# Kernel optimization log

Hardware: AMD Instinct MI355X
Metric: run time of the kernel (lower is better)

The kernel has to match this reference:

```python
import jax, jax.numpy as jnp
import numpy as np

B, E, C = 512, 512, 100000
S, M, LAMDA, ALPHA = 30.0, 0.35, 0.01, 0.5  # s, m, lamda from init; ALPHA = args.alpha (center lr)
EPS = 1e-6


def setup_inputs() -> dict:
    key = jax.random.key(0)
    k1, k2, k3, k4 = jax.random.split(key, 4)
    embedding = jax.random.normal(k1, (B, E), dtype=jnp.float32)
    weights = jax.random.normal(k2, (C, E), dtype=jnp.float32)  # kaiming-init classifier weights
    centers = jax.random.normal(k3, (C, E), dtype=jnp.float32)  # class centers buffer
    label = jax.random.randint(k4, (B,), 0, C, dtype=jnp.int64)
    return {"embedding": embedding, "weights": weights, "centers": centers, "label": label}


def reference(embedding, weights, centers, label):
    rows = jnp.arange(B)
    # LMCL (CosFace) logits: cosine similarity via L2-normalized features and weights
    emb_n = embedding / jnp.linalg.norm(embedding, axis=1, keepdims=True)
    w_n = weights / jnp.linalg.norm(weights, axis=1, keepdims=True)
    logits = jnp.einsum('be,ce->bc', emb_n, w_n)            # [B, C]
    # subtract margin m at the target class, then scale by s
    m_logits = S * logits.at[rows, label].add(-M)
    logp = jax.nn.log_softmax(m_logits, axis=1)
    lmcl_loss = -jnp.mean(logp[rows, label])
    # top-1 precision (%)
    prec = jnp.mean((jnp.argmax(m_logits, axis=1) == label).astype(jnp.float32)) * 100.0
    # center loss: MSE between features and their class centers (centers treated as constant)
    centers_batch = centers[label]                           # [B, E] gather
    center_loss = jnp.mean((embedding - centers_batch) ** 2)
    # center update: scatter-subtract mean-normalized diff (replaces the python loop)
    counts = jnp.zeros((C,), dtype=jnp.float32).at[label].add(1.0)
    appear = counts[label]                                   # [B]
    diff = ALPHA * (centers_batch - embedding) / (appear[:, None] + EPS)
    new_centers = centers.at[label].add(-diff)
    total_loss = lmcl_loss + LAMDA * center_loss
    return prec, total_loss, new_centers
```

## Files before the change

### kernel.cpp

```cpp
#include <hip/hip_runtime.h>
#include <cstdint>
#include <cstddef>

#define B_ROWS 512
#define E_DIM  512
#define C_CLS  100000
#define NT     782

#define S_SC    30.0f
#define M_MRG   0.35f
#define LAMBDA_ 0.01f
#define ALPHA_  0.5f
#define EPS_    1e-6f

#define GBN    128
#define GSTEPS 16

typedef __attribute__((ext_vector_type(8))) short bf16x8;
typedef __attribute__((ext_vector_type(4))) float f32x4;

static_assert((size_t)NT * GBN >= C_CLS, "tile count");

constexpr size_t WS_PSUM  = 0;
constexpr size_t WS_PMAX  = WS_PSUM + (size_t)NT * B_ROWS * 4;
constexpr size_t WS_CLOSS = WS_PMAX + (size_t)NT * B_ROWS * 4;
constexpr size_t WS_EMBN  = WS_CLOSS + 512;
constexpr size_t WS_COSL  = WS_EMBN + (size_t)B_ROWS * E_DIM * 2;
constexpr size_t WS_CNT   = WS_COSL + 2048;
constexpr size_t WS_RSUM  = WS_CNT + 2048;
constexpr size_t WS_RMAX  = WS_RSUM + 2048;

__device__ __forceinline__ unsigned short f2bf(float f) {
    unsigned u = __float_as_uint(f);
    u += 0x7fffu + ((u >> 16) & 1u);
    return (unsigned short)(u >> 16);
}
__device__ __forceinline__ unsigned fkey(float f) {
    unsigned u = __float_as_uint(f);
    return (u & 0x80000000u) ? ~u : (u | 0x80000000u);
}
__device__ __forceinline__ float unkey(unsigned k) {
    unsigned u = (k & 0x80000000u) ? (k ^ 0x80000000u) : ~k;
    return __uint_as_float(u);
}
__device__ __forceinline__ float waveReduceSum(float v) {
#pragma unroll
    for (int d = 1; d < 64; d <<= 1) v += __shfl_xor(v, d, 64);
    return v;
}
__device__ __forceinline__ unsigned waveReduceMax(unsigned v) {
#pragma unroll
    for (int d = 1; d < 64; d <<= 1) { unsigned o = __shfl_xor(v, d, 64); v = o > v ? o : v; }
    return v;
}
__device__ __forceinline__ float blockReduceSum256(float v, float* s4) {
    v = waveReduceSum(v);
    int w = threadIdx.x >> 6;
    if ((threadIdx.x & 63) == 0) s4[w] = v;
    __syncthreads();
    float r = s4[0] + s4[1] + s4[2] + s4[3];
    __syncthreads();
    return r;
}


__global__ __launch_bounds__(256) void prep_stats(const float* __restrict__ emb,
                                                  const float* __restrict__ W,
                                                  const float* __restrict__ centers,
                                                  const int* __restrict__ label,
                                                  unsigned short* __restrict__ embn,
                                                  float* __restrict__ cosl,
                                                  float* __restrict__ cntf,
                                                  float* __restrict__ closs) {
    __shared__ float s4[4];
    int b = blockIdx.x, t = threadIdx.x;
    int lab = label[b];
    float2 e2 = *(const float2*)(emb     + (size_t)b   * E_DIM + t * 2);
    float2 w2 = *(const float2*)(W       + (size_t)lab * E_DIM + t * 2);
    float2 c2 = *(const float2*)(centers + (size_t)lab * E_DIM + t * 2);
    float ssq = e2.x * e2.x + e2.y * e2.y;
    float d   = e2.x * w2.x + e2.y * w2.y;
    float wss = w2.x * w2.x + w2.y * w2.y;
    float dx = e2.x - c2.x, dy = e2.y - c2.y;
    float sq  = dx * dx + dy * dy;
    float cn = ((label[t] == lab) ? 1.f : 0.f) + ((label[t + 256] == lab) ? 1.f : 0.f);
    ssq = blockReduceSum256(ssq, s4);
    d   = blockReduceSum256(d,   s4);
    wss = blockReduceSum256(wss, s4);
    sq  = blockReduceSum256(sq,  s4);
    cn  = blockReduceSum256(cn,  s4);
    float inv = 1.0f / sqrtf(ssq);
    ushort2 o; o.x = f2bf(e2.x * inv); o.y = f2bf(e2.y * inv);
    *(ushort2*)(embn + (size_t)b * E_DIM + t * 2) = o;
    if (t == 0) {
        cosl[b] = d * inv / sqrtf(wss);
        cntf[b] = cn;
        atomicAdd(closs, sq);
    }
}

__global__ __launch_bounds__(512, 1) void gemm_fused(const unsigned short* __restrict__ embn,
                                                     const float* __restrict__ W,
                                                     const int* __restrict__ label,
                                                     float* __restrict__ psum,
                                                     unsigned* __restrict__ pmax,
                                                     const float* __restrict__ centers,
                                                     float* __restrict__ outC,
                                                     unsigned* __restrict__ ctr) {
    __shared__ __align__(16) unsigned short sB[2][GBN * 32];
    __shared__ int      sLab[B_ROWS];
    __shared__ float    sInv[GBN];
    __shared__ unsigned sChunk;

    const int tid  = threadIdx.x;
    const int lane = tid & 63, wave = tid >> 6;
    const int wm = wave >> 1, wn = wave & 1;
    const int q = lane >> 4, lm = lane & 15;
    const int n0 = blockIdx.x * GBN;

    sLab[tid & (B_ROWS - 1)] = label[tid & (B_ROWS - 1)];

    const int brow = tid >> 2;
    const int bl   = tid & 3;
    int brg = n0 + brow; if (brg >= C_CLS) brg = 0;
    const float* bsrc = W + (size_t)brg * E_DIM + bl * 8;
    const int bphys = bl ^ ((brow >> 1) & 3);
    unsigned short* bwr = &sB[0][brow * 32 + bphys * 8];

    const unsigned short* aP[8];
#pragma unroll
    for (int i = 0; i < 8; ++i)
        aP[i] = embn + (size_t)(wm * 128 + i * 16 + lm) * E_DIM + q * 8;

    const unsigned short* brd[4];
#pragma unroll
    for (int j = 0; j < 4; ++j) {
        int row = wn * 64 + j * 16 + lm;
        brd[j] = &sB[0][row * 32 + (q ^ ((row >> 1) & 3)) * 8];
    }

    f32x4 acc[8][4];
#pragma unroll
    for (int i = 0; i < 8; ++i)
#pragma unroll
        for (int j = 0; j < 4; ++j) acc[i][j] = (f32x4){0.f, 0.f, 0.f, 0.f};

    float ss = 0.f;
    f32x4 bA0, bA1, bB0, bB1;

    bA0 = *(const f32x4*)(bsrc + 0);
    bA1 = *(const f32x4*)(bsrc + 4);
    bB0 = *(const f32x4*)(bsrc + 32);
    bB1 = *(const f32x4*)(bsrc + 36);
    {
        ss += bA0.x*bA0.x + bA0.y*bA0.y + bA0.z*bA0.z + bA0.w*bA0.w
            + bA1.x*bA1.x + bA1.y*bA1.y + bA1.z*bA1.z + bA1.w*bA1.w;
        bf16x8 o;
        o[0] = (short)f2bf(bA0.x); o[1] = (short)f2bf(bA0.y);
        o[2] = (short)f2bf(bA0.z); o[3] = (short)f2bf(bA0.w);
        o[4] = (short)f2bf(bA1.x); o[5] = (short)f2bf(bA1.y);
        o[6] = (short)f2bf(bA1.z); o[7] = (short)f2bf(bA1.w);
        *(bf16x8*)bwr = o;
    }
    asm volatile("s_waitcnt lgkmcnt(0)" ::: "memory");
    __builtin_amdgcn_sched_barrier(0);
    __builtin_amdgcn_s_barrier();

#define STEP(T, WR0, WR1, LD0, LD1)                                             \
    {                                                                           \
        const int t_ = (T);                                                     \
        bf16x8 af[8];                                                           \
        _Pragma("unroll")                                                       \
        for (int i = 0; i < 8; ++i)                                             \
            af[i] = *(const bf16x8*)(aP[i] + t_ * 32);                          \
        if (t_ + 2 < GSTEPS) {                                                  \
            LD0 = *(const f32x4*)(bsrc + (t_ + 2) * 32);                        \
            LD1 = *(const f32x4*)(bsrc + (t_ + 2) * 32 + 4);                    \
        }                                                                       \
        if (t_ + 1 < GSTEPS) {                                                  \
            ss += WR0.x*WR0.x + WR0.y*WR0.y + WR0.z*WR0.z + WR0.w*WR0.w         \
                + WR1.x*WR1.x + WR1.y*WR1.y + WR1.z*WR1.z + WR1.w*WR1.w;        \
            bf16x8 o;                                                           \
            o[0] = (short)f2bf(WR0.x); o[1] = (short)f2bf(WR0.y);               \
            o[2] = (short)f2bf(WR0.z); o[3] = (short)f2bf(WR0.w);               \
            o[4] = (short)f2bf(WR1.x); o[5] = (short)f2bf(WR1.y);               \
            o[6] = (short)f2bf(WR1.z); o[7] = (short)f2bf(WR1.w);               \
            *(bf16x8*)(bwr + ((t_ + 1) & 1) * 4096) = o;                        \
        }                                                                       \
        bf16x8 bfr[4];                                                          \
        _Pragma("unroll")                                                       \
        for (int j = 0; j < 4; ++j)                                             \
            bfr[j] = *(const bf16x8*)(brd[j] + (t_ & 1) * 4096);                \
        _Pragma("unroll")                                                       \
        for (int i = 0; i < 8; ++i)                                             \
            _Pragma("unroll")                                                   \
            for (int j = 0; j < 4; ++j)                                         \
                acc[i][j] = __builtin_amdgcn_mfma_f32_16x16x32_bf16(af[i], bfr[j], acc[i][j], 0, 0, 0); \
        __builtin_amdgcn_sched_barrier(0);                                      \
        asm volatile("s_waitcnt lgkmcnt(0)" ::: "memory");                      \
        __builtin_amdgcn_sched_barrier(0);                                      \
        __builtin_amdgcn_s_barrier();                                           \
    }

#pragma unroll
    for (int tt = 0; tt < GSTEPS; tt += 2) {
        STEP(tt,     bB0, bB1, bA0, bA1);
        STEP(tt + 1, bA0, bA1, bB0, bB1);
    }
#undef STEP

    ss += __shfl_xor(ss, 1, 64);
    ss += __shfl_xor(ss, 2, 64);
    if ((tid & 3) == 0) sInv[brow] = rsqrtf(fmaxf(ss, 1e-30f));
    __syncthreads();

    float inv_j[4];
#pragma unroll
    for (int j = 0; j < 4; ++j) inv_j[j] = sInv[wn * 64 + j * 16 + lm];

    const size_t pbase = (size_t)blockIdx.x * B_ROWS;
#pragma unroll
    for (int i = 0; i < 8; ++i) {
#pragma unroll
        for (int r = 0; r < 4; ++r) {
            int row = wm * 128 + i * 16 + q * 4 + r;
            int lab = sLab[row];
            float sum = 0.f, mx = -1e30f;
#pragma unroll
            for (int j = 0; j < 4; ++j) {
                int col = n0 + wn * 64 + j * 16 + lm;
                float v = S_SC * acc[i][j][r] * inv_j[j];
                if (col < C_CLS && col != lab) {
                    sum += __expf(v - 30.0f);
                    mx = fmaxf(mx, v);
                }
            }
#pragma unroll
            for (int d = 1; d < 16; d <<= 1) {
                sum += __shfl_xor(sum, d, 64);
                mx = fmaxf(mx, __shfl_xor(mx, d, 64));
            }
            if (lm == 0) {
                atomicAdd(&psum[pbase + row], sum);
                atomicMax(&pmax[pbase + row], fkey(mx));
            }
        }
    }

    constexpr size_t N4 = ((size_t)C_CLS * E_DIM - 2) / 4;
    constexpr unsigned NCHUNK = (unsigned)((N4 + 4095) / 4096);
    const float2* s2 = (const float2*)(centers + 2);
    float4* d4 = (float4*)(outC + 2);
    for (;;) {
        if (tid == 0) sChunk = atomicAdd(ctr, 1u);
        __syncthreads();
        unsigned c = sChunk;
        __syncthreads();
        if (c >= NCHUNK) break;
        size_t g0 = (size_t)c * 4096;
#pragma unroll
        for (int u = 0; u < 8; ++u) {
            size_t g = g0 + (size_t)u * 512 + tid;
            if (g < N4) {
                float2 a = s2[2 * g], b = s2[2 * g + 1];
                d4[g] = make_float4(a.x, a.y, b.x, b.y);
            }
        }
        if (c == 0 && tid == 0) {
            *(float2*)outC = *(const float2*)centers;
            constexpr size_t t0 = 2 + 4 * N4;
            *(float2*)(outC + t0) = *(const float2*)(centers + t0);
        }
    }
}

__global__ __launch_bounds__(256) void row_reduce(const float* __restrict__ psum,
                                                  const unsigned* __restrict__ pmax,
                                                  float* __restrict__ rsum,
                                                  float* __restrict__ rmax) {
    __shared__ float s4[4];
    __shared__ unsigned m4[4];
    int b = blockIdx.x, t = threadIdx.x;
    float s = 0.f; unsigned mk = 0u;
    for (int nt = t; nt < NT; nt += 256) {
        s += psum[(size_t)nt * B_ROWS + b];
        unsigned k = pmax[(size_t)nt * B_ROWS + b];
        mk = k > mk ? k : mk;
    }
    s = waveReduceSum(s);
    mk = waveReduceMax(mk);
    int w = t >> 6;
    if ((t & 63) == 0) { s4[w] = s; m4[w] = mk; }
    __syncthreads();
    if (t == 0) {
        rsum[b] = s4[0] + s4[1] + s4[2] + s4[3];
        unsigned m = m4[0];
#pragma unroll
        for (int i = 1; i < 4; ++i) m = m4[i] > m ? m4[i] : m;
        rmax[b] = unkey(m);
    }
}

__global__ __launch_bounds__(256) void finalize(const float* __restrict__ cosl,
                                                const float* __restrict__ rsum,
                                                const float* __restrict__ rmax,
                                                const float* __restrict__ closs,
                                                float* __restrict__ out) {
    __shared__ float s4[4];
    int t = threadIdx.x;
    float lsum = 0.f, msum = 0.f;
    for (int b = t; b < B_ROWS; b += 256) {
        float lv = S_SC * (cosl[b] - M_MRG);
        float tot = rsum[b] + __expf(lv - 30.0f);
        lsum += (logf(tot) + 30.0f) - lv;
        msum += (lv > rmax[b]) ? 1.0f : 0.0f;
    }
    lsum = blockReduceSum256(lsum, s4);
    msum = blockReduceSum256(msum, s4);
    if (t == 0) {
        out[0] = msum * (100.0f / (float)B_ROWS);
        out[1] = lsum * (1.0f / (float)B_ROWS)
               + LAMBDA_ * closs[0] * (1.0f / ((float)B_ROWS * (float)E_DIM));
    }
}

__global__ __launch_bounds__(256) void scatter_upd(const float* __restrict__ emb,
                                                   const float* __restrict__ centers,
                                                   const int* __restrict__ label,
                                                   const float* __restrict__ cntf,
                                                   float* __restrict__ outC) {
    int b = blockIdx.x, t = threadIdx.x;
    int lab = label[b];
    float sc = ALPHA_ / (cntf[b] + EPS_);
    for (int c = t; c < E_DIM; c += 256) {
        float add = sc * (emb[(size_t)b * E_DIM + c] - centers[(size_t)lab * E_DIM + c]);
        atomicAdd(outC + (size_t)lab * E_DIM + c, add);
    }
}

extern "C" void kernel_launch(void* const* d_in, const int* in_sizes, int n_in,
                              void* d_out, int out_size, void* d_ws, size_t ws_size,
                              hipStream_t stream) {
    const float* emb     = (const float*)d_in[0];
    const float* W       = (const float*)d_in[1];
    const float* centers = (const float*)d_in[2];
    const int*   label   = (const int*)d_in[3];
    float* out = (float*)d_out;
    char* ws = (char*)d_ws;

    float*          psum = (float*)(ws + WS_PSUM);
    unsigned*       pmax = (unsigned*)(ws + WS_PMAX);
    float*          closs = (float*)(ws + WS_CLOSS);
    unsigned*       ctr  = (unsigned*)(ws + WS_CLOSS + 8);
    unsigned short* embn = (unsigned short*)(ws + WS_EMBN);
    float*          cosl = (float*)(ws + WS_COSL);
    float*          cntf = (float*)(ws + WS_CNT);
    float*          rsum = (float*)(ws + WS_RSUM);
    float*          rmax = (float*)(ws + WS_RMAX);

    (void)hipMemsetAsync(ws, 0, WS_CLOSS + 512, stream);

    prep_stats<<<B_ROWS, 256, 0, stream>>>(emb, W, centers, label, embn, cosl, cntf, closs);
    gemm_fused<<<NT, 512, 0, stream>>>(embn, W, label, psum, pmax, centers, out + 2, ctr);
    row_reduce<<<B_ROWS, 256, 0, stream>>>(psum, pmax, rsum, rmax);
    finalize<<<1, 256, 0, stream>>>(cosl, rsum, rmax, closs, out);
    scatter_upd<<<B_ROWS, 256, 0, stream>>>(emb, centers, label, cntf, out + 2);
}
```

Measured before the change: 617.4 us.

## Stage A operand through LDS with async global_load_lds triple buffering

```diff
diff --git a/kernel.cpp b/kernel.cpp
--- a/kernel.cpp
+++ b/kernel.cpp
@@ -15,6 +15,8 @@
 
 #define GBN    128
 #define GSTEPS 16
+#define ASLOT  (512 * 32)
+#define BSLOT  (128 * 32)
 
 typedef __attribute__((ext_vector_type(8))) short bf16x8;
 typedef __attribute__((ext_vector_type(4))) float f32x4;
@@ -61,6 +63,11 @@
     float r = s4[0] + s4[1] + s4[2] + s4[3];
     __syncthreads();
     return r;
+}
+__device__ __forceinline__ void g2l16(const void* g, void* l) {
+    __builtin_amdgcn_global_load_lds(
+        (const __attribute__((address_space(1))) unsigned int*)g,
+        (__attribute__((address_space(3))) unsigned int*)l, 16, 0, 0);
 }
 
 
@@ -105,12 +112,11 @@
                                                      float* __restrict__ psum,
                                                      unsigned* __restrict__ pmax,
                                                      const float* __restrict__ centers,
-                                                     float* __restrict__ outC,
-                                                     unsigned* __restrict__ ctr) {
-    __shared__ __align__(16) unsigned short sB[2][GBN * 32];
-    __shared__ int      sLab[B_ROWS];
-    __shared__ float    sInv[GBN];
-    __shared__ unsigned sChunk;
+                                                     float* __restrict__ outC) {
+    __shared__ __align__(16) unsigned short sA[3 * ASLOT];
+    __shared__ __align__(16) unsigned short sBl[2 * BSLOT];
+    __shared__ int   sLab[B_ROWS];
+    __shared__ float sInv[GBN];
 
     const int tid  = threadIdx.x;
     const int lane = tid & 63, wave = tid >> 6;
@@ -118,26 +124,30 @@
     const int q = lane >> 4, lm = lane & 15;
     const int n0 = blockIdx.x * GBN;
 
-    sLab[tid & (B_ROWS - 1)] = label[tid & (B_ROWS - 1)];
+    sLab[tid] = label[tid];
+
+    const int swz = (tid & 3) ^ ((tid >> 3) & 3);
+    int aOff[4];
+#pragma unroll
+    for (int j = 0; j < 4; ++j)
+        aOff[j] = (j * 128 + (tid >> 2)) * E_DIM + swz * 8;
 
     const int brow = tid >> 2;
     const int bl   = tid & 3;
     int brg = n0 + brow; if (brg >= C_CLS) brg = 0;
     const float* bsrc = W + (size_t)brg * E_DIM + bl * 8;
     const int bphys = bl ^ ((brow >> 1) & 3);
-    unsigned short* bwr = &sB[0][brow * 32 + bphys * 8];
-
-    const unsigned short* aP[8];
+    unsigned short* bwr = &sBl[brow * 32 + bphys * 8];
+
+    const int pq8 = (q ^ ((lm >> 1) & 3)) * 8;
+    int aRd[8];
 #pragma unroll
     for (int i = 0; i < 8; ++i)
-        aP[i] = embn + (size_t)(wm * 128 + i * 16 + lm) * E_DIM + q * 8;
-
-    const unsigned short* brd[4];
-#pragma unroll
-    for (int j = 0; j < 4; ++j) {
-        int row = wn * 64 + j * 16 + lm;
-        brd[j] = &sB[0][row * 32 + (q ^ ((row >> 1) & 3)) * 8];
-    }
+        aRd[i] = (wm * 128 + i * 16 + lm) * 32 + pq8;
+    int bRd[4];
+#pragma unroll
+    for (int j = 0; j < 4; ++j)
+        bRd[j] = (wn * 64 + j * 16 + lm) * 32 + pq8;
 
     f32x4 acc[8][4];
 #pragma unroll
@@ -148,6 +158,12 @@
     float ss = 0.f;
     f32x4 bA0, bA1, bB0, bB1;
 
+#pragma unroll
+    for (int j = 0; j < 4; ++j)
+        g2l16(embn + aOff[j], &sA[0 * ASLOT + (j * 512 + wave * 64) * 8]);
+#pragma unroll
+    for (int j = 0; j < 4; ++j)
+        g2l16(embn + aOff[j] + 32, &sA[1 * ASLOT + (j * 512 + wave * 64) * 8]);
     bA0 = *(const f32x4*)(bsrc + 0);
     bA1 = *(const f32x4*)(bsrc + 4);
     bB0 = *(const f32x4*)(bsrc + 32);
@@ -169,14 +185,30 @@
 #define STEP(T, WR0, WR1, LD0, LD1)                                             \
     {                                                                           \
         const int t_ = (T);                                                     \
-        bf16x8 af[8];                                                           \
-        _Pragma("unroll")                                                       \
-        for (int i = 0; i < 8; ++i)                                             \
-            af[i] = *(const bf16x8*)(aP[i] + t_ * 32);                          \
         if (t_ + 2 < GSTEPS) {                                                  \
+            _Pragma("unroll")                                                   \
+            for (int j = 0; j < 4; ++j)                                         \
+                g2l16(embn + aOff[j] + (t_ + 2) * 32,                           \
+                      &sA[((t_ + 2) % 3) * ASLOT + (j * 512 + wave * 64) * 8]); \
             LD0 = *(const f32x4*)(bsrc + (t_ + 2) * 32);                        \
             LD1 = *(const f32x4*)(bsrc + (t_ + 2) * 32 + 4);                    \
         }                                                                       \
+        __builtin_amdgcn_sched_barrier(0);                                      \
+        {                                                                       \
+            const unsigned short* sa = &sA[(t_ % 3) * ASLOT];                   \
+            const unsigned short* sb = &sBl[(t_ & 1) * BSLOT];                  \
+            bf16x8 af[8], bfr[4];                                               \
+            _Pragma("unroll")                                                   \
+            for (int i = 0; i < 8; ++i) af[i] = *(const bf16x8*)(sa + aRd[i]);  \
+            _Pragma("unroll")                                                   \
+            for (int j = 0; j < 4; ++j) bfr[j] = *(const bf16x8*)(sb + bRd[j]); \
+            _Pragma("unroll")                                                   \
+            for (int i = 0; i < 8; ++i)                                         \
+                _Pragma("unroll")                                               \
+                for (int j = 0; j < 4; ++j)                                     \
+                    acc[i][j] = __builtin_amdgcn_mfma_f32_16x16x32_bf16(af[i], bfr[j], acc[i][j], 0, 0, 0); \
+        }                                                                       \
+        __builtin_amdgcn_sched_barrier(0);                                      \
         if (t_ + 1 < GSTEPS) {                                                  \
             ss += WR0.x*WR0.x + WR0.y*WR0.y + WR0.z*WR0.z + WR0.w*WR0.w         \
                 + WR1.x*WR1.x + WR1.y*WR1.y + WR1.z*WR1.z + WR1.w*WR1.w;        \
@@ -185,21 +217,17 @@
             o[2] = (short)f2bf(WR0.z); o[3] = (short)f2bf(WR0.w);               \
             o[4] = (short)f2bf(WR1.x); o[5] = (short)f2bf(WR1.y);               \
             o[6] = (short)f2bf(WR1.z); o[7] = (short)f2bf(WR1.w);               \
-            *(bf16x8*)(bwr + ((t_ + 1) & 1) * 4096) = o;                        \
+            *(bf16x8*)(bwr + ((t_ + 1) & 1) * BSLOT) = o;                       \
         }                                                                       \
-        bf16x8 bfr[4];                                                          \
-        _Pragma("unroll")                                                       \
-        for (int j = 0; j < 4; ++j)                                             \
-            bfr[j] = *(const bf16x8*)(brd[j] + (t_ & 1) * 4096);                \
-        _Pragma("unroll")                                                       \
-        for (int i = 0; i < 8; ++i)                                             \
-            _Pragma("unroll")                                                   \
-            for (int j = 0; j < 4; ++j)                                         \
-                acc[i][j] = __builtin_amdgcn_mfma_f32_16x16x32_bf16(af[i], bfr[j], acc[i][j], 0, 0, 0); \
         __builtin_amdgcn_sched_barrier(0);                                      \
-        asm volatile("s_waitcnt lgkmcnt(0)" ::: "memory");                      \
-        __builtin_amdgcn_sched_barrier(0);                                      \
-        __builtin_amdgcn_s_barrier();                                           \
+        if (t_ < GSTEPS - 1) {                                                  \
+            if (t_ + 2 < GSTEPS)                                                \
+                asm volatile("s_waitcnt vmcnt(6) lgkmcnt(0)" ::: "memory");     \
+            else                                                                \
+                asm volatile("s_waitcnt vmcnt(0) lgkmcnt(0)" ::: "memory");     \
+            __builtin_amdgcn_sched_barrier(0);                                  \
+            __builtin_amdgcn_s_barrier();                                       \
+        }                                                                       \
     }
 
 #pragma unroll
@@ -248,29 +276,21 @@
     }
 
     constexpr size_t N4 = ((size_t)C_CLS * E_DIM - 2) / 4;
-    constexpr unsigned NCHUNK = (unsigned)((N4 + 4095) / 4096);
     const float2* s2 = (const float2*)(centers + 2);
     float4* d4 = (float4*)(outC + 2);
-    for (;;) {
-        if (tid == 0) sChunk = atomicAdd(ctr, 1u);
-        __syncthreads();
-        unsigned c = sChunk;
-        __syncthreads();
-        if (c >= NCHUNK) break;
-        size_t g0 = (size_t)c * 4096;
-#pragma unroll
-        for (int u = 0; u < 8; ++u) {
-            size_t g = g0 + (size_t)u * 512 + tid;
-            if (g < N4) {
-                float2 a = s2[2 * g], b = s2[2 * g + 1];
-                d4[g] = make_float4(a.x, a.y, b.x, b.y);
-            }
+    const size_t base = (size_t)blockIdx.x * 16384;
+#pragma unroll 4
+    for (int u = 0; u < 32; ++u) {
+        size_t g = base + (size_t)u * 512 + tid;
+        if (g < N4) {
+            float2 a = s2[2 * g], b = s2[2 * g + 1];
+            d4[g] = make_float4(a.x, a.y, b.x, b.y);
         }
-        if (c == 0 && tid == 0) {
-            *(float2*)outC = *(const float2*)centers;
-            constexpr size_t t0 = 2 + 4 * N4;
-            *(float2*)(outC + t0) = *(const float2*)(centers + t0);
-        }
+    }
+    if (blockIdx.x == 0 && tid == 0) {
+        *(float2*)outC = *(const float2*)centers;
+        constexpr size_t t0 = 2 + 4 * N4;
+        *(float2*)(outC + t0) = *(const float2*)(centers + t0);
     }
 }
 
@@ -351,7 +371,6 @@
     float*          psum = (float*)(ws + WS_PSUM);
     unsigned*       pmax = (unsigned*)(ws + WS_PMAX);
     float*          closs = (float*)(ws + WS_CLOSS);
-    unsigned*       ctr  = (unsigned*)(ws + WS_CLOSS + 8);
     unsigned short* embn = (unsigned short*)(ws + WS_EMBN);
     float*          cosl = (float*)(ws + WS_COSL);
     float*          cntf = (float*)(ws + WS_CNT);
@@ -361,7 +380,7 @@
     (void)hipMemsetAsync(ws, 0, WS_CLOSS + 512, stream);
 
     prep_stats<<<B_ROWS, 256, 0, stream>>>(emb, W, centers, label, embn, cosl, cntf, closs);
-    gemm_fused<<<NT, 512, 0, stream>>>(embn, W, label, psum, pmax, centers, out + 2, ctr);
+    gemm_fused<<<NT, 512, 0, stream>>>(embn, W, label, psum, pmax, centers, out + 2);
     row_reduce<<<B_ROWS, 256, 0, stream>>>(psum, pmax, rsum, rmax);
     finalize<<<1, 256, 0, stream>>>(cosl, rsum, rmax, closs, out);
     scatter_upd<<<B_ROWS, 256, 0, stream>>>(emb, centers, label, cntf, out + 2);
```

Result: faster. 595.2 us (-3.6%).
